# Performance work log

Measured on AMD Instinct MI355X. Metric: run time of the kernel, lower is better.

## Reference

```python
import jax, jax.numpy as jnp
import numpy as np
from jax import lax

B, T, D, N = 64, 4096, 256, 64


def setup_inputs() -> dict:
    key = jax.random.key(0)
    ks = jax.random.split(key, 3)
    return {
        "x": jax.random.normal(ks[0], (B, T, D), dtype=jnp.float32),
        "mask": jnp.ones((B, T), dtype=bool),
        "W": jax.random.normal(ks[1], (D, N), dtype=jnp.float32) * (1.0 / np.sqrt(D)),
        "b": jnp.zeros((N,), dtype=jnp.float32),
        "trans": jax.random.normal(ks[2], (N, N), dtype=jnp.float32) * 0.1,
        "left_boundary": jnp.zeros((N,), dtype=jnp.float32),
        "right_boundary": jnp.zeros((N,), dtype=jnp.float32),
    }


def _viterbi_decode(potentials, lens, trans):
    # potentials: [B, T, N]; lens: [B] int32; trans: [N, N]
    Tt = potentials.shape[1]

    def fwd_step(state, inp):
        pot_t, t = inp  # pot_t: [B, N], t scalar time index (1..T-1)
        scores = state[:, :, None] + trans[None, :, :]        # [B, N_prev, N_cur]
        bp = jnp.argmax(scores, axis=1).astype(jnp.int32)      # [B, N]
        new_state = pot_t + jnp.max(scores, axis=1)            # [B, N]
        valid = (t < lens)[:, None]                            # carry state past length
        return jnp.where(valid, new_state, state), bp

    pots_t = jnp.swapaxes(potentials, 0, 1)  # [T, B, N]
    final_state, bps = lax.scan(fwd_step, pots_t[0], (pots_t[1:], jnp.arange(1, Tt)))
    last_tag = jnp.argmax(final_state, axis=1).astype(jnp.int32)  # [B]

    def bwd_step(tag, inp):
        bp, t = inp  # bp: [B, N] backpointers for time t+1; t in 0..T-2
        prev = jnp.take_along_axis(bp, tag[:, None], axis=1)[:, 0]
        new_tag = jnp.where(t < lens - 1, prev, last_tag)
        return new_tag, new_tag

    _, tags = lax.scan(bwd_step, last_tag, (bps, jnp.arange(Tt - 1)), reverse=True)
    # tags: [T-1, B], position t holds decoded tag at time t
    decoded = jnp.concatenate([tags.T, last_tag[:, None]], axis=1)  # [B, T]
    return decoded


def reference(x, mask, W, b, trans, left_boundary, right_boundary):
    # projection (use_kernel=True)
    pot = jnp.einsum("btd,dn->btn", x, W) + b  # [B, T, N]
    # boundary potentials (use_boundary=True): added at fixed first/last timestep
    pot = pot.at[:, 0, :].add(left_boundary)
    pot = pot.at[:, -1, :].add(right_boundary)
    lens = jnp.sum(mask.astype(jnp.int32), axis=1)  # [B]
    decoded = _viterbi_decode(pot, lens, trans)
    return decoded, pot, lens, trans
```

## Files before the change

kernel.cpp:

```cpp
#include <hip/hip_runtime.h>

#define B_ 64
#define T_ 4096
#define D_ 256
#define N_ 64

typedef float f32x16 __attribute__((ext_vector_type(16)));

__global__ __launch_bounds__(64) void k_misc(const unsigned char* __restrict__ mask,
                                             const float* __restrict__ trans,
                                             float* __restrict__ out_lens,
                                             float* __restrict__ out_trans,
                                             int* __restrict__ lens_i) {
  int blk = blockIdx.x, lane = threadIdx.x;
  if (blk < B_) {
    int probe = (int)mask[0] + (int)mask[1] + (int)mask[2] + (int)mask[3];
    int cnt = 0;
    if (probe >= 2) {
      const unsigned char* row = mask + (size_t)blk * T_;
      for (int i = lane; i < T_; i += 64) cnt += row[i] ? 1 : 0;
    } else {
      const int* rowi = (const int*)mask + (size_t)blk * T_;
      for (int i = lane; i < T_; i += 64) cnt += rowi[i] ? 1 : 0;
    }
    #pragma unroll
    for (int off = 32; off > 0; off >>= 1) cnt += __shfl_down(cnt, off, 64);
    if (lane == 0) { out_lens[blk] = (float)cnt; lens_i[blk] = cnt; }
  } else {
    int base = (blk - B_) * 1024;
    for (int i = lane; i < 1024; i += 64) out_trans[base + i] = trans[base + i];
  }
}

__global__ __launch_bounds__(256, 4) void k_gemm(const float* __restrict__ x,
                                                 const float* __restrict__ W,
                                                 const float* __restrict__ bias,
                                                 const float* __restrict__ lb,
                                                 const float* __restrict__ rb,
                                                 float* __restrict__ pot) {
  int wave = (blockIdx.x * blockDim.x + threadIdx.x) >> 6;
  int wave_u = __builtin_amdgcn_readfirstlane(wave);
  int lane = threadIdx.x & 63;
  long row0 = (long)wave_u * 16;

  float bv = bias[lane];
  float lbv = lb[lane];
  float rbv = rb[lane];

  float acc[16];
  #pragma unroll
  for (int r = 0; r < 16; ++r) {
    int t = (int)((row0 + r) & (T_ - 1));
    float a = bv;
    if (t == 0)      a += lbv;
    if (t == T_ - 1) a += rbv;
    acc[r] = a;
  }

  const float* xb = x + (size_t)row0 * D_;

  #pragma unroll
  for (int c = 0; c < 4; ++c) {
    int d0 = c * 64;
    float w[64];
    #pragma unroll
    for (int k = 0; k < 64; ++k) w[k] = W[(d0 + k) * N_ + lane];
    #pragma unroll
    for (int r = 0; r < 16; ++r) {
      const f32x16* xr = reinterpret_cast<const f32x16*>(xb + r * D_ + d0);
      #pragma unroll
      for (int q = 0; q < 4; ++q) {
        f32x16 xv = xr[q];
        #pragma unroll
        for (int j = 0; j < 16; ++j) acc[r] += xv[j] * w[q * 16 + j];
      }
    }
  }

  #pragma unroll
  for (int r = 0; r < 16; ++r) pot[(row0 + r) * N_ + lane] = acc[r];
}

#define FWD_STEP(TIDX, PREG)                                                      \
  {                                                                               \
    float pot_t = PREG;                                                           \
    int tp = (TIDX) + 4; if (tp > T_ - 1) tp = T_ - 1;                            \
    PREG = pb[(size_t)tp * N_ + lane];                                            \
    float m[64];                                                                  \
    _Pragma("unroll")                                                             \
    for (int g = 0; g < 16; ++g) {                                                \
      float4 s4 = st4v[g];                                                        \
      float2 ca = make_float2(s4.x, s4.y) + t2[2 * g];                            \
      float2 cb = make_float2(s4.z, s4.w) + t2[2 * g + 1];                        \
      m[4 * g + 0] = ca.x; m[4 * g + 1] = ca.y;                                   \
      m[4 * g + 2] = cb.x; m[4 * g + 3] = cb.y;                                   \
    }                                                                             \
    float r1[22];                                                                 \
    _Pragma("unroll")                                                             \
    for (int i = 0; i < 21; ++i)                                                  \
      r1[i] = fmaxf(fmaxf(m[3 * i], m[3 * i + 1]), m[3 * i + 2]);                 \
    r1[21] = m[63];                                                               \
    float r2[8];                                                                  \
    _Pragma("unroll")                                                             \
    for (int i = 0; i < 7; ++i)                                                   \
      r2[i] = fmaxf(fmaxf(r1[3 * i], r1[3 * i + 1]), r1[3 * i + 2]);              \
    r2[7] = r1[21];                                                               \
    float r3a = fmaxf(fmaxf(r2[0], r2[1]), r2[2]);                                \
    float r3b = fmaxf(fmaxf(r2[3], r2[4]), r2[5]);                                \
    float r3c = fmaxf(r2[6], r2[7]);                                              \
    float best = fmaxf(fmaxf(r3a, r3b), r3c);                                     \
    float ns = pot_t + best;                                                      \
    state = ((TIDX) < len_b) ? ns : state;                                        \
    sb[(size_t)(TIDX) * N_ + lane] = state;                                       \
    __builtin_amdgcn_wave_barrier();                                              \
    st[lane] = state;                                                             \
    __builtin_amdgcn_wave_barrier();                                              \
  }

__global__ __launch_bounds__(64, 1) void k_fwd_states(const float* __restrict__ pot,
                                                      const float* __restrict__ trans,
                                                      const int* __restrict__ lens_i,
                                                      float* __restrict__ states,
                                                      float* __restrict__ fstate) {
  int b = blockIdx.x, lane = threadIdx.x;
  __shared__ float4 st4v[16];
  float* st = (float*)st4v;

  float2 t2[32];
  #pragma unroll
  for (int p = 0; p < 32; ++p)
    t2[p] = make_float2(trans[(2 * p) * N_ + lane], trans[(2 * p + 1) * N_ + lane]);

  const float* pb = pot + (size_t)b * T_ * N_;
  float* sb = states + (size_t)b * T_ * N_;
  int len_b = lens_i[b];

  float state = pb[lane];
  st[lane] = state;
  sb[lane] = state;
  __builtin_amdgcn_wave_barrier();

  float p0 = pb[1 * N_ + lane];
  float p1 = pb[2 * N_ + lane];
  float p2 = pb[3 * N_ + lane];
  float p3 = pb[4 * N_ + lane];

  int t = 1;
  for (; t + 3 <= T_ - 1; t += 4) {
    FWD_STEP(t + 0, p0);
    FWD_STEP(t + 1, p1);
    FWD_STEP(t + 2, p2);
    FWD_STEP(t + 3, p3);
  }
  FWD_STEP(t + 0, p0);
  FWD_STEP(t + 1, p1);
  FWD_STEP(t + 2, p2);

  fstate[b * N_ + lane] = state;
}

#define BP_CHUNK 64
__global__ __launch_bounds__(64, 2) void k_bp(const float* __restrict__ states,
                                              const float* __restrict__ trans,
                                              unsigned char* __restrict__ bp) {
  int nchunk = T_ / BP_CHUNK;
  int b = blockIdx.x / nchunk;
  int chunk = blockIdx.x - b * nchunk;
  int lane = threadIdx.x;

  float tcol[64];
  #pragma unroll
  for (int p = 0; p < 64; ++p) tcol[p] = trans[p * N_ + lane];

  int t0 = chunk * BP_CHUNK;
  int tstart = (t0 == 0) ? 1 : t0;
  int tend = t0 + BP_CHUNK;

  for (int t = tstart; t < tend; ++t) {
    const f32x16* sr = reinterpret_cast<const f32x16*>(states + ((size_t)b * T_ + (t - 1)) * N_);
    f32x16 s0 = sr[0], s1 = sr[1], s2 = sr[2], s3 = sr[3];

    float c[64];
    #pragma unroll
    for (int j = 0; j < 16; ++j) {
      c[j]      = s0[j] + tcol[j];
      c[16 + j] = s1[j] + tcol[16 + j];
      c[32 + j] = s2[j] + tcol[32 + j];
      c[48 + j] = s3[j] + tcol[48 + j];
    }

    float r1[22];
    #pragma unroll
    for (int i = 0; i < 21; ++i) r1[i] = fmaxf(fmaxf(c[3 * i], c[3 * i + 1]), c[3 * i + 2]);
    r1[21] = c[63];
    float r2[8];
    #pragma unroll
    for (int i = 0; i < 7; ++i) r2[i] = fmaxf(fmaxf(r1[3 * i], r1[3 * i + 1]), r1[3 * i + 2]);
    r2[7] = r1[21];
    float r3a = fmaxf(fmaxf(r2[0], r2[1]), r2[2]);
    float r3b = fmaxf(fmaxf(r2[3], r2[4]), r2[5]);
    float r3c = fmaxf(r2[6], r2[7]);
    float best = fmaxf(fmaxf(r3a, r3b), r3c);

    int bpi = 63;
    #pragma unroll
    for (int p = 62; p >= 0; --p) bpi = (c[p] == best) ? p : bpi;

    bp[((size_t)b * T_ + t) * N_ + lane] = (unsigned char)bpi;
  }
}

__global__ __launch_bounds__(64, 1) void k_bwd(const unsigned char* __restrict__ bp,
                                               const float* __restrict__ fstate,
                                               const int* __restrict__ lens_i,
                                               float* __restrict__ decoded) {
  int b = blockIdx.x, lane = threadIdx.x;

  __shared__ float fv[64];
  __shared__ int sh_tag;
  fv[lane] = fstate[b * N_ + lane];
  __syncthreads();
  if (lane == 0) {
    float best = fv[0]; int tg = 0;
    for (int i = 1; i < 64; ++i) if (fv[i] > best) { best = fv[i]; tg = i; }
    sh_tag = tg;
  }
  __syncthreads();
  int last_tag = sh_tag;
  int len_b = lens_i[b];

  const unsigned char* bpb = bp + (size_t)b * T_ * N_;
  float* dec = decoded + (size_t)b * T_;

  int tag = last_tag;
  if (lane == 0) dec[T_ - 1] = (float)last_tag;

  const int G = 16;
  int bufA[G], bufB[G];
  const int k0 = T_ - 1;
  #pragma unroll
  for (int i = 0; i < G; ++i) bufA[i] = (int)bpb[(size_t)(k0 - i) * N_ + lane];

  const int nrows = T_ - 1;
  const int groups = nrows / G;

  for (int g = 0; g < groups; ++g) {
    int kn = k0 - G * (g + 1);
    #pragma unroll
    for (int i = 0; i < G; ++i)
      bufB[i] = (kn - i >= 1) ? (int)bpb[(size_t)(kn - i) * N_ + lane] : 0;

    int kbase = k0 - G * g;
    #pragma unroll
    for (int i = 0; i < G; ++i) {
      int k = kbase - i;
      int prev = __shfl(bufA[i], tag, 64);
      int t = k - 1;
      tag = (t < len_b - 1) ? prev : last_tag;
      if (lane == 0) dec[t] = (float)tag;
    }
    #pragma unroll
    for (int i = 0; i < G; ++i) bufA[i] = bufB[i];
  }

  int kbase = k0 - G * groups;
  #pragma unroll
  for (int i = 0; i < G; ++i) {
    int k = kbase - i;
    if (k >= 1) {
      int prev = __shfl(bufA[i], tag, 64);
      int t = k - 1;
      tag = (t < len_b - 1) ? prev : last_tag;
      if (lane == 0) dec[t] = (float)tag;
    }
  }
}

extern "C" void kernel_launch(void* const* d_in, const int* in_sizes, int n_in,
                              void* d_out, int out_size, void* d_ws, size_t ws_size,
                              hipStream_t stream) {
  const float* x            = (const float*)d_in[0];
  const unsigned char* mask = (const unsigned char*)d_in[1];
  const float* W            = (const float*)d_in[2];
  const float* bias         = (const float*)d_in[3];
  const float* trans        = (const float*)d_in[4];
  const float* lb           = (const float*)d_in[5];
  const float* rb           = (const float*)d_in[6];

  float* out         = (float*)d_out;
  float* out_decoded = out;
  float* out_pot     = out + (size_t)B_ * T_;
  float* out_lens    = out_pot + (size_t)B_ * T_ * N_;
  float* out_trans   = out_lens + B_;

  const size_t bp_bytes     = (size_t)B_ * T_ * N_;
  const size_t fstate_off   = bp_bytes;
  const size_t lens_off     = fstate_off + (size_t)B_ * N_ * 4;
  const size_t states_off   = lens_off + 256;
  const size_t states_bytes = (size_t)B_ * T_ * N_ * 4;

  unsigned char* bp = (unsigned char*)d_ws;
  float* fstate     = (float*)((char*)d_ws + fstate_off);
  int*   lens_i     = (int*)((char*)d_ws + lens_off);
  float* states     = (float*)((char*)d_ws + states_off);

  k_misc<<<68, 64, 0, stream>>>(mask, trans, out_lens, out_trans, lens_i);
  k_gemm<<<(B_ * T_) / 64, 256, 0, stream>>>(x, W, bias, lb, rb, out_pot);
  k_fwd_states<<<B_, 64, 0, stream>>>(out_pot, trans, lens_i, states, fstate);
  k_bp<<<B_ * (T_ / BP_CHUNK), 64, 0, stream>>>(states, trans, bp);
  k_bwd<<<B_, 64, 0, stream>>>(bp, fstate, lens_i, out_decoded);
}
```

Baseline: 1.759 ms.

## Fuse forward Viterbi and backpointer kernels via LDS ring, stage GEMM x in LDS

The forward-state scan and backpointer computation now run in one kernel per batch. Wave 0 runs the recurrence and writes each state into a 64-entry shared-memory ring. Three worker waves compute argmax backpointers concurrently, synchronising through volatile LDS flags. This removes the full states buffer round trip through global memory and one kernel launch. The GEMM also stages x rows into LDS, and the backward pass uses scalar readlane with a larger prefetch group. The spin-wait flag protocol adds risk of ordering or memory-visibility bugs, and of stalls when the producer waits on the consumers.

```diff
diff --git a/kernel.cpp b/kernel.cpp
--- a/kernel.cpp
+++ b/kernel.cpp
@@ -32,16 +32,25 @@
   }
 }
 
-__global__ __launch_bounds__(256, 4) void k_gemm(const float* __restrict__ x,
+__global__ __launch_bounds__(256, 2) void k_gemm(const float* __restrict__ x,
                                                  const float* __restrict__ W,
                                                  const float* __restrict__ bias,
                                                  const float* __restrict__ lb,
                                                  const float* __restrict__ rb,
                                                  float* __restrict__ pot) {
-  int wave = (blockIdx.x * blockDim.x + threadIdx.x) >> 6;
-  int wave_u = __builtin_amdgcn_readfirstlane(wave);
-  int lane = threadIdx.x & 63;
-  long row0 = (long)wave_u * 16;
+  __shared__ float xs[64 * D_];
+  int tid = threadIdx.x;
+  int wid = tid >> 6, lane = tid & 63;
+  size_t row0 = (size_t)blockIdx.x * 64;
+
+  const float* xb = x + row0 * D_;
+  #pragma unroll
+  for (int i = 0; i < 16; ++i) {
+    int r = wid * 16 + i;
+    float4 v = *reinterpret_cast<const float4*>(xb + (size_t)r * D_ + lane * 4);
+    *reinterpret_cast<float4*>(&xs[r * D_ + lane * 4]) = v;
+  }
+  __syncthreads();
 
   float bv = bias[lane];
   float lbv = lb[lane];
@@ -50,35 +59,35 @@
   float acc[16];
   #pragma unroll
   for (int r = 0; r < 16; ++r) {
-    int t = (int)((row0 + r) & (T_ - 1));
+    int t = (int)((row0 + wid * 16 + r) & (T_ - 1));
     float a = bv;
     if (t == 0)      a += lbv;
     if (t == T_ - 1) a += rbv;
     acc[r] = a;
   }
 
-  const float* xb = x + (size_t)row0 * D_;
-
   #pragma unroll
   for (int c = 0; c < 4; ++c) {
-    int d0 = c * 64;
     float w[64];
     #pragma unroll
-    for (int k = 0; k < 64; ++k) w[k] = W[(d0 + k) * N_ + lane];
+    for (int k = 0; k < 64; ++k) w[k] = W[(size_t)(c * 64 + k) * N_ + lane];
     #pragma unroll
     for (int r = 0; r < 16; ++r) {
-      const f32x16* xr = reinterpret_cast<const f32x16*>(xb + r * D_ + d0);
-      #pragma unroll
-      for (int q = 0; q < 4; ++q) {
-        f32x16 xv = xr[q];
-        #pragma unroll
-        for (int j = 0; j < 16; ++j) acc[r] += xv[j] * w[q * 16 + j];
+      const float4* xr = reinterpret_cast<const float4*>(&xs[(wid * 16 + r) * D_ + c * 64]);
+      #pragma unroll
+      for (int q = 0; q < 16; ++q) {
+        float4 xv = xr[q];
+        acc[r] += xv.x * w[q * 4 + 0];
+        acc[r] += xv.y * w[q * 4 + 1];
+        acc[r] += xv.z * w[q * 4 + 2];
+        acc[r] += xv.w * w[q * 4 + 3];
       }
     }
   }
 
   #pragma unroll
-  for (int r = 0; r < 16; ++r) pot[(row0 + r) * N_ + lane] = acc[r];
+  for (int r = 0; r < 16; ++r)
+    pot[(row0 + wid * 16 + r) * N_ + lane] = acc[r];
 }
 
 #define FWD_STEP(TIDX, PREG)                                                      \
@@ -86,10 +95,11 @@
     float pot_t = PREG;                                                           \
     int tp = (TIDX) + 4; if (tp > T_ - 1) tp = T_ - 1;                            \
     PREG = pb[(size_t)tp * N_ + lane];                                            \
+    const float4* rs = ring4 + (((TIDX) - 1) & 63) * 16;                          \
     float m[64];                                                                  \
     _Pragma("unroll")                                                             \
     for (int g = 0; g < 16; ++g) {                                                \
-      float4 s4 = st4v[g];                                                        \
+      float4 s4 = rs[g];                                                          \
       float2 ca = make_float2(s4.x, s4.y) + t2[2 * g];                            \
       float2 cb = make_float2(s4.z, s4.w) + t2[2 * g + 1];                        \
       m[4 * g + 0] = ca.x; m[4 * g + 1] = ca.y;                                   \
@@ -111,102 +121,119 @@
     float best = fmaxf(fmaxf(r3a, r3b), r3c);                                     \
     float ns = pot_t + best;                                                      \
     state = ((TIDX) < len_b) ? ns : state;                                        \
-    sb[(size_t)(TIDX) * N_ + lane] = state;                                       \
-    __builtin_amdgcn_wave_barrier();                                              \
-    st[lane] = state;                                                             \
-    __builtin_amdgcn_wave_barrier();                                              \
-  }
-
-__global__ __launch_bounds__(64, 1) void k_fwd_states(const float* __restrict__ pot,
-                                                      const float* __restrict__ trans,
-                                                      const int* __restrict__ lens_i,
-                                                      float* __restrict__ states,
-                                                      float* __restrict__ fstate) {
-  int b = blockIdx.x, lane = threadIdx.x;
-  __shared__ float4 st4v[16];
-  float* st = (float*)st4v;
-
-  float2 t2[32];
-  #pragma unroll
-  for (int p = 0; p < 32; ++p)
-    t2[p] = make_float2(trans[(2 * p) * N_ + lane], trans[(2 * p + 1) * N_ + lane]);
+    ringf[(((TIDX) & 63) << 6) + lane] = state;                                   \
+    __asm__ volatile("" ::: "memory");                                            \
+    if (lane == 0) *flag_v = (TIDX);                                              \
+    __asm__ volatile("" ::: "memory");                                            \
+  }
+
+__global__ __launch_bounds__(256, 1) void k_fwd_bp(const float* __restrict__ pot,
+                                                   const float* __restrict__ trans,
+                                                   const int* __restrict__ lens_i,
+                                                   unsigned char* __restrict__ bp,
+                                                   float* __restrict__ fstate) {
+  __shared__ float ringf[64 * 64];
+  __shared__ int sync_flag;
+  __shared__ int ccs[3];
+
+  int b = blockIdx.x;
+  int tid = threadIdx.x;
+  int wid = tid >> 6, lane = tid & 63;
+
+  volatile int* flag_v = &sync_flag;
+  volatile int* cc_v = ccs;
+
+  const float4* ring4 = reinterpret_cast<const float4*>(ringf);
+
+  if (tid == 0) { sync_flag = 0; ccs[0] = 0; ccs[1] = 0; ccs[2] = 0; }
 
   const float* pb = pot + (size_t)b * T_ * N_;
-  float* sb = states + (size_t)b * T_ * N_;
+  unsigned char* bpb = bp + (size_t)b * T_ * N_;
   int len_b = lens_i[b];
 
-  float state = pb[lane];
-  st[lane] = state;
-  sb[lane] = state;
-  __builtin_amdgcn_wave_barrier();
-
-  float p0 = pb[1 * N_ + lane];
-  float p1 = pb[2 * N_ + lane];
-  float p2 = pb[3 * N_ + lane];
-  float p3 = pb[4 * N_ + lane];
-
-  int t = 1;
-  for (; t + 3 <= T_ - 1; t += 4) {
+  if (wid == 0) {
+    float state0 = pb[lane];
+    ringf[lane] = state0;
+  }
+  __syncthreads();
+
+  if (wid == 0) {
+    float2 t2[32];
+    #pragma unroll
+    for (int p = 0; p < 32; ++p)
+      t2[p] = make_float2(trans[(2 * p) * N_ + lane], trans[(2 * p + 1) * N_ + lane]);
+
+    float state = ringf[lane];
+
+    float p0 = pb[1 * N_ + lane];
+    float p1 = pb[2 * N_ + lane];
+    float p2 = pb[3 * N_ + lane];
+    float p3 = pb[4 * N_ + lane];
+
+    int t = 1;
+    for (; t + 3 <= T_ - 1; t += 4) {
+      if (((t - 1) & 31) == 0) {
+        while (true) {
+          int m0 = cc_v[0], m1 = cc_v[1], m2 = cc_v[2];
+          int mn = m0 < m1 ? m0 : m1; mn = mn < m2 ? mn : m2;
+          if (mn >= t - 32) break;
+          __builtin_amdgcn_s_sleep(1);
+        }
+      }
+      FWD_STEP(t + 0, p0);
+      FWD_STEP(t + 1, p1);
+      FWD_STEP(t + 2, p2);
+      FWD_STEP(t + 3, p3);
+    }
     FWD_STEP(t + 0, p0);
     FWD_STEP(t + 1, p1);
     FWD_STEP(t + 2, p2);
-    FWD_STEP(t + 3, p3);
-  }
-  FWD_STEP(t + 0, p0);
-  FWD_STEP(t + 1, p1);
-  FWD_STEP(t + 2, p2);
-
-  fstate[b * N_ + lane] = state;
-}
-
-#define BP_CHUNK 64
-__global__ __launch_bounds__(64, 2) void k_bp(const float* __restrict__ states,
-                                              const float* __restrict__ trans,
-                                              unsigned char* __restrict__ bp) {
-  int nchunk = T_ / BP_CHUNK;
-  int b = blockIdx.x / nchunk;
-  int chunk = blockIdx.x - b * nchunk;
-  int lane = threadIdx.x;
-
-  float tcol[64];
-  #pragma unroll
-  for (int p = 0; p < 64; ++p) tcol[p] = trans[p * N_ + lane];
-
-  int t0 = chunk * BP_CHUNK;
-  int tstart = (t0 == 0) ? 1 : t0;
-  int tend = t0 + BP_CHUNK;
-
-  for (int t = tstart; t < tend; ++t) {
-    const f32x16* sr = reinterpret_cast<const f32x16*>(states + ((size_t)b * T_ + (t - 1)) * N_);
-    f32x16 s0 = sr[0], s1 = sr[1], s2 = sr[2], s3 = sr[3];
-
-    float c[64];
-    #pragma unroll
-    for (int j = 0; j < 16; ++j) {
-      c[j]      = s0[j] + tcol[j];
-      c[16 + j] = s1[j] + tcol[16 + j];
-      c[32 + j] = s2[j] + tcol[32 + j];
-      c[48 + j] = s3[j] + tcol[48 + j];
-    }
-
-    float r1[22];
-    #pragma unroll
-    for (int i = 0; i < 21; ++i) r1[i] = fmaxf(fmaxf(c[3 * i], c[3 * i + 1]), c[3 * i + 2]);
-    r1[21] = c[63];
-    float r2[8];
-    #pragma unroll
-    for (int i = 0; i < 7; ++i) r2[i] = fmaxf(fmaxf(r1[3 * i], r1[3 * i + 1]), r1[3 * i + 2]);
-    r2[7] = r1[21];
-    float r3a = fmaxf(fmaxf(r2[0], r2[1]), r2[2]);
-    float r3b = fmaxf(fmaxf(r2[3], r2[4]), r2[5]);
-    float r3c = fmaxf(r2[6], r2[7]);
-    float best = fmaxf(fmaxf(r3a, r3b), r3c);
-
-    int bpi = 63;
-    #pragma unroll
-    for (int p = 62; p >= 0; --p) bpi = (c[p] == best) ? p : bpi;
-
-    bp[((size_t)b * T_ + t) * N_ + lane] = (unsigned char)bpi;
+
+    fstate[b * N_ + lane] = state;
+  } else {
+    int w = wid - 1;
+    float tcol[64];
+    #pragma unroll
+    for (int p = 0; p < 64; ++p) tcol[p] = trans[p * N_ + lane];
+
+    for (int t = 1 + w; t <= T_ - 1; t += 3) {
+      while (*flag_v < t - 1) __builtin_amdgcn_s_sleep(1);
+      __asm__ volatile("" ::: "memory");
+
+      const float4* rs = ring4 + ((t - 1) & 63) * 16;
+      float c[64];
+      #pragma unroll
+      for (int g = 0; g < 16; ++g) {
+        float4 s4 = rs[g];
+        c[4 * g + 0] = s4.x + tcol[4 * g + 0];
+        c[4 * g + 1] = s4.y + tcol[4 * g + 1];
+        c[4 * g + 2] = s4.z + tcol[4 * g + 2];
+        c[4 * g + 3] = s4.w + tcol[4 * g + 3];
+      }
+
+      float r1[22];
+      #pragma unroll
+      for (int i = 0; i < 21; ++i) r1[i] = fmaxf(fmaxf(c[3 * i], c[3 * i + 1]), c[3 * i + 2]);
+      r1[21] = c[63];
+      float r2[8];
+      #pragma unroll
+      for (int i = 0; i < 7; ++i) r2[i] = fmaxf(fmaxf(r1[3 * i], r1[3 * i + 1]), r1[3 * i + 2]);
+      r2[7] = r1[21];
+      float r3a = fmaxf(fmaxf(r2[0], r2[1]), r2[2]);
+      float r3b = fmaxf(fmaxf(r2[3], r2[4]), r2[5]);
+      float r3c = fmaxf(r2[6], r2[7]);
+      float best = fmaxf(fmaxf(r3a, r3b), r3c);
+
+      int bpi = 63;
+      #pragma unroll
+      for (int p = 62; p >= 0; --p) bpi = (c[p] == best) ? p : bpi;
+
+      bpb[(size_t)t * N_ + lane] = (unsigned char)bpi;
+
+      __asm__ volatile("" ::: "memory");
+      if (lane == 0) cc_v[w] = t;
+    }
+    if (lane == 0) cc_v[w] = T_;
   }
 }
 
@@ -226,16 +253,16 @@
     sh_tag = tg;
   }
   __syncthreads();
-  int last_tag = sh_tag;
+  int s_last = __builtin_amdgcn_readfirstlane(sh_tag);
   int len_b = lens_i[b];
 
   const unsigned char* bpb = bp + (size_t)b * T_ * N_;
   float* dec = decoded + (size_t)b * T_;
 
-  int tag = last_tag;
-  if (lane == 0) dec[T_ - 1] = (float)last_tag;
-
-  const int G = 16;
+  int s_tag = s_last;
+  if (lane == 0) dec[T_ - 1] = (float)s_last;
+
+  const int G = 32;
   int bufA[G], bufB[G];
   const int k0 = T_ - 1;
   #pragma unroll
@@ -254,10 +281,10 @@
     #pragma unroll
     for (int i = 0; i < G; ++i) {
       int k = kbase - i;
-      int prev = __shfl(bufA[i], tag, 64);
+      int prev = __builtin_amdgcn_readlane(bufA[i], s_tag);
       int t = k - 1;
-      tag = (t < len_b - 1) ? prev : last_tag;
-      if (lane == 0) dec[t] = (float)tag;
+      s_tag = (t < len_b - 1) ? prev : s_last;
+      if (lane == 0) dec[t] = (float)s_tag;
     }
     #pragma unroll
     for (int i = 0; i < G; ++i) bufA[i] = bufB[i];
@@ -268,10 +295,10 @@
   for (int i = 0; i < G; ++i) {
     int k = kbase - i;
     if (k >= 1) {
-      int prev = __shfl(bufA[i], tag, 64);
+      int prev = __builtin_amdgcn_readlane(bufA[i], s_tag);
       int t = k - 1;
-      tag = (t < len_b - 1) ? prev : last_tag;
-      if (lane == 0) dec[t] = (float)tag;
+      s_tag = (t < len_b - 1) ? prev : s_last;
+      if (lane == 0) dec[t] = (float)s_tag;
     }
   }
 }
@@ -293,20 +320,16 @@
   float* out_lens    = out_pot + (size_t)B_ * T_ * N_;
   float* out_trans   = out_lens + B_;
 
-  const size_t bp_bytes     = (size_t)B_ * T_ * N_;
-  const size_t fstate_off   = bp_bytes;
-  const size_t lens_off     = fstate_off + (size_t)B_ * N_ * 4;
-  const size_t states_off   = lens_off + 256;
-  const size_t states_bytes = (size_t)B_ * T_ * N_ * 4;
+  const size_t bp_bytes   = (size_t)B_ * T_ * N_;
+  const size_t fstate_off = bp_bytes;
+  const size_t lens_off   = fstate_off + (size_t)B_ * N_ * 4;
 
   unsigned char* bp = (unsigned char*)d_ws;
   float* fstate     = (float*)((char*)d_ws + fstate_off);
   int*   lens_i     = (int*)((char*)d_ws + lens_off);
-  float* states     = (float*)((char*)d_ws + states_off);
 
   k_misc<<<68, 64, 0, stream>>>(mask, trans, out_lens, out_trans, lens_i);
   k_gemm<<<(B_ * T_) / 64, 256, 0, stream>>>(x, W, bias, lb, rb, out_pot);
-  k_fwd_states<<<B_, 64, 0, stream>>>(out_pot, trans, lens_i, states, fstate);
-  k_bp<<<B_ * (T_ / BP_CHUNK), 64, 0, stream>>>(states, trans, bp);
+  k_fwd_bp<<<B_, 256, 0, stream>>>(out_pot, trans, lens_i, bp, fstate);
   k_bwd<<<B_, 64, 0, stream>>>(bp, fstate, lens_i, out_decoded);
 }
```

Measured after the change: 1.774 ms. Within noise of the previous version (+0.9%).
